# Performance work log

Measured on AMD Instinct MI355X. Metric: run time of the kernel, lower is better.

## Reference

```python
import jax, jax.numpy as jnp
import numpy as np

# DLMLayer (breadth=2) forward, soft/dense path.
# Group arities: 0 (nullary [B,C0]), 1 (unary [B,n,C1]), 2 (binary [B,n,n,C2]).
# Per group i: concat [Expand(inputs[i-1]), inputs[i], Reduce(inputs[i+1])],
# then Permutation(i) (concat over i! axis permutations), then logic MLP
# (Linear -> sigmoid) over the channel dim. exclude_self masks the diagonal
# in the binary->unary reduction (max filled with 0, min filled with 1,
# valid for probabilistic truth values in [0,1]).

def setup_inputs() -> dict:
    key = jax.random.key(0)
    ks = jax.random.split(key, 9)
    B, n, C = 16, 128, 64
    x0 = jax.random.uniform(ks[0], (B, 8), dtype=jnp.float32)
    x1 = jax.random.uniform(ks[1], (B, n, C), dtype=jnp.float32)
    x2 = jax.random.uniform(ks[2], (B, n, n, C), dtype=jnp.float32)
    # current_dim per group: i=0: 8 + 2*64 = 136 ; i=1: 8 + 64 + 2*64 = 200 (1!=1)
    # i=2: (64 + 64) * 2! = 256
    W0 = jax.random.normal(ks[3], (136, C), dtype=jnp.float32) * 0.1
    W1 = jax.random.normal(ks[4], (200, C), dtype=jnp.float32) * 0.1
    W2 = jax.random.normal(ks[5], (256, C), dtype=jnp.float32) * 0.1
    b0 = jnp.zeros((C,), jnp.float32)
    b1 = jnp.zeros((C,), jnp.float32)
    b2 = jnp.zeros((C,), jnp.float32)
    return {"x0": x0, "x1": x1, "x2": x2, "W0": W0, "b0": b0,
            "W1": W1, "b1": b1, "W2": W2, "b2": b2}


def reference(x0, x1, x2, W0, b0, W1, b1, W2, b2):
    B, n, C = x1.shape
    # ---- group 0 (nullary): input x0 + reduce(x1) over the object axis ----
    r1 = jnp.concatenate([x1.max(axis=1), x1.min(axis=1)], axis=-1)  # [B, 2C]
    f0 = jnp.concatenate([x0, r1], axis=-1)                          # [B, 136]
    out0 = jax.nn.sigmoid(f0 @ W0 + b0)                              # [B, C]
    # ---- group 1 (unary): expand x0, input x1, reduce x2 (exclude self) ----
    e0 = jnp.broadcast_to(x0[:, None, :], (B, n, x0.shape[-1]))      # [B, n, 8]
    diag = jnp.eye(n, dtype=bool)[None, :, :, None]                  # [1, n, n, 1]
    rmax = jnp.where(diag, 0.0, x2).max(axis=2)                      # [B, n, C]
    rmin = jnp.where(diag, 1.0, x2).min(axis=2)                      # [B, n, C]
    f1 = jnp.concatenate([e0, x1, rmax, rmin], axis=-1)              # [B, n, 200]
    out1 = jax.nn.sigmoid(f1 @ W1 + b1)                              # [B, n, C]
    # ---- group 2 (binary): expand x1, input x2, permute axes (1,2) ----
    e1 = jnp.broadcast_to(x1[:, :, None, :], (B, n, n, C))           # [B, n, n, C]
    g = jnp.concatenate([e1, x2], axis=-1)                           # [B, n, n, 2C]
    f2 = jnp.concatenate([g, jnp.swapaxes(g, 1, 2)], axis=-1)        # [B, n, n, 4C]
    out2 = jax.nn.sigmoid(f2 @ W2 + b2)                              # [B, n, n, C]
    return (out0, out1, out2)
```

## Files before the change

### kernel.cpp

```cpp
#include <hip/hip_runtime.h>
#include <hip/hip_bf16.h>
#include <cstdint>


#define NDIM 128
#define CDIM 64

typedef float f32x4 __attribute__((ext_vector_type(4)));
typedef short s16x8 __attribute__((ext_vector_type(8)));

__device__ __forceinline__ unsigned short f2bf(float f) {
    union { float f; unsigned int u; } v; v.f = f;
    unsigned int u = v.u;
    return (unsigned short)((u + 0x7FFFu + ((u >> 16) & 1u)) >> 16);
}
__device__ __forceinline__ float sigmoidf_(float x) {
    return 1.0f / (1.0f + __expf(-x));
}
__device__ __forceinline__ uint2 pk4(float4 v) {
    unsigned lo, hi;
    asm("v_cvt_pk_bf16_f32 %0, %1, %2" : "=v"(lo) : "v"(v.x), "v"(v.y));
    asm("v_cvt_pk_bf16_f32 %0, %1, %2" : "=v"(hi) : "v"(v.z), "v"(v.w));
    uint2 r; r.x = lo; r.y = hi; return r;
}

__global__ __launch_bounds__(256) void k_prep(const float* __restrict__ x0,
        const float* __restrict__ x1, const float* __restrict__ W0,
        const float* __restrict__ b0, const float* __restrict__ W2,
        const float* __restrict__ b2, float* __restrict__ PA,
        float* __restrict__ PB, unsigned short* __restrict__ WT,
        float* __restrict__ out0) {
    int bb = blockIdx.x;
    int t = threadIdx.x;
    if (bb < 512) {
        int u = t >> 6, c = t & 63;
        int blk = bb * 4 + u;
        __shared__ float xv[4][64];
        xv[u][c] = x1[blk * 64 + c];
        float accA = b2[c];
        float accB = 0.f;
#pragma unroll 8
        for (int k = 0; k < 64; ++k) {
            float xk = xv[u][k];
            accA += xk * W2[k * 64 + c];
            accB += xk * W2[(128 + k) * 64 + c];
        }
        PA[blk * 64 + c] = accA;
        PB[blk * 64 + c] = accB;
    } else if (bb < 544) {
        int idx = (bb - 512) * 256 + t;
        int n = idx >> 7, k = idx & 127;
        int row = (k < 64) ? (64 + k) : (128 + k);
        WT[idx] = f2bf(W2[row * 64 + n]);
    } else {
        int b = bb - 544;
        int lane = t & 63, w = t >> 6;
        int q = lane & 15;
        int jq = lane >> 4;
        __shared__ float pw[4][64], pn[4][64], f0[136], spart[4][64];
        f32x4 mx = {-1e30f, -1e30f, -1e30f, -1e30f};
        f32x4 mn = {1e30f, 1e30f, 1e30f, 1e30f};
#pragma unroll
        for (int p = 0; p < 8; ++p) {
            int j = (w * 4 + jq) + 16 * p;
            float4 v = *reinterpret_cast<const float4*>(
                x1 + ((size_t)(b * 128 + j)) * 64 + q * 4);
            mx.x = fmaxf(mx.x, v.x); mx.y = fmaxf(mx.y, v.y);
            mx.z = fmaxf(mx.z, v.z); mx.w = fmaxf(mx.w, v.w);
            mn.x = fminf(mn.x, v.x); mn.y = fminf(mn.y, v.y);
            mn.z = fminf(mn.z, v.z); mn.w = fminf(mn.w, v.w);
        }
#pragma unroll
        for (int d = 16; d <= 32; d <<= 1) {
            mx.x = fmaxf(mx.x, __shfl_xor(mx.x, d)); mx.y = fmaxf(mx.y, __shfl_xor(mx.y, d));
            mx.z = fmaxf(mx.z, __shfl_xor(mx.z, d)); mx.w = fmaxf(mx.w, __shfl_xor(mx.w, d));
            mn.x = fminf(mn.x, __shfl_xor(mn.x, d)); mn.y = fminf(mn.y, __shfl_xor(mn.y, d));
            mn.z = fminf(mn.z, __shfl_xor(mn.z, d)); mn.w = fminf(mn.w, __shfl_xor(mn.w, d));
        }
        if (lane < 16) {
            *reinterpret_cast<f32x4*>(&pw[w][lane * 4]) = mx;
            *reinterpret_cast<f32x4*>(&pn[w][lane * 4]) = mn;
        }
        __syncthreads();
        if (t < 64) {
            int c = t;
            float M = fmaxf(fmaxf(pw[0][c], pw[1][c]), fmaxf(pw[2][c], pw[3][c]));
            float m = fminf(fminf(pn[0][c], pn[1][c]), fminf(pn[2][c], pn[3][c]));
            f0[8 + c] = M; f0[72 + c] = m;
            if (c < 8) f0[c] = x0[b * 8 + c];
        }
        __syncthreads();
        {
            int g = t >> 6, c = t & 63;
            float acc = 0.f;
#pragma unroll
            for (int k = g * 34; k < g * 34 + 34; ++k) acc += f0[k] * W0[k * 64 + c];
            spart[g][c] = acc;
        }
        __syncthreads();
        if (t < 64) {
            int c = t;
            out0[b * 64 + c] = sigmoidf_(
                spart[0][c] + spart[1][c] + spart[2][c] + spart[3][c] + b0[c]);
        }
    }
}

__global__ __launch_bounds__(128) void k_main(const float* __restrict__ x2,
        const unsigned short* __restrict__ WT,
        const float* __restrict__ PA, const float* __restrict__ PB,
        float* __restrict__ pmax_ws, float* __restrict__ pmin_ws,
        float* __restrict__ out2) {
    int bid = blockIdx.x;
    int blk = bid >> 1, half = bid & 1;
    int b = blk >> 7, i = blk & 127;
    int j0 = half << 6;
    int t = threadIdx.x;
    int lane = t & 63, w = t >> 6;
    int jq = lane >> 4;
    int cc = (lane & 15) * 4;

    __shared__ __align__(16) unsigned short Ald[64 * 128];

    const float* xaSrc = x2 + (size_t)blk * (NDIM * CDIM);

    float4 va[8];
#pragma unroll
    for (int p = 0; p < 8; ++p) {
        int jl = 32 * w + p * 4 + jq;
        va[p] = *reinterpret_cast<const float4*>(xaSrc + (j0 + jl) * 64 + cc);
    }
    f32x4 mx = {0.f, 0.f, 0.f, 0.f}, mn = {1.f, 1.f, 1.f, 1.f};
#pragma unroll
    for (int p = 0; p < 8; ++p) {
        int jl = 32 * w + p * 4 + jq;
        bool ok = (j0 + jl != i);
        mx.x = fmaxf(mx.x, ok ? va[p].x : 0.0f); mx.y = fmaxf(mx.y, ok ? va[p].y : 0.0f);
        mx.z = fmaxf(mx.z, ok ? va[p].z : 0.0f); mx.w = fmaxf(mx.w, ok ? va[p].w : 0.0f);
        mn.x = fminf(mn.x, ok ? va[p].x : 1.0f); mn.y = fminf(mn.y, ok ? va[p].y : 1.0f);
        mn.z = fminf(mn.z, ok ? va[p].z : 1.0f); mn.w = fminf(mn.w, ok ? va[p].w : 1.0f);
        uint2 u = pk4(va[p]);
        *reinterpret_cast<uint2*>(&Ald[jl * 128 + (cc ^ ((jl & 7) << 3))]) = u;
    }

    float4 vb[8];
#pragma unroll
    for (int p = 0; p < 8; ++p) {
        int jl = 32 * w + p * 4 + jq;
        vb[p] = *reinterpret_cast<const float4*>(
            x2 + ((size_t)((b * 128 + j0 + jl) * 128 + i)) * 64 + cc);
    }

#pragma unroll
    for (int d = 16; d <= 32; d <<= 1) {
        mx.x = fmaxf(mx.x, __shfl_xor(mx.x, d)); mx.y = fmaxf(mx.y, __shfl_xor(mx.y, d));
        mx.z = fmaxf(mx.z, __shfl_xor(mx.z, d)); mx.w = fmaxf(mx.w, __shfl_xor(mx.w, d));
        mn.x = fminf(mn.x, __shfl_xor(mn.x, d)); mn.y = fminf(mn.y, __shfl_xor(mn.y, d));
        mn.z = fminf(mn.z, __shfl_xor(mn.z, d)); mn.w = fminf(mn.w, __shfl_xor(mn.w, d));
    }
    if (lane < 16) {
        int slot = blk * 4 + half * 2 + w;
        *reinterpret_cast<f32x4*>(&pmax_ws[slot * 64 + cc]) = mx;
        *reinterpret_cast<f32x4*>(&pmin_ws[slot * 64 + cc]) = mn;
    }

    s16x8 bf01[2][4];
#pragma unroll
    for (int ks = 0; ks < 2; ++ks)
#pragma unroll
        for (int nt = 0; nt < 4; ++nt) {
            int n = nt * 16 + (lane & 15);
            bf01[ks][nt] = *reinterpret_cast<const s16x8*>(WT + n * 128 + ks * 32 + jq * 8);
        }

    f32x4 acc[2][4];
#pragma unroll
    for (int m = 0; m < 2; ++m)
#pragma unroll
        for (int nt = 0; nt < 4; ++nt) acc[m][nt] = (f32x4){0.f, 0.f, 0.f, 0.f};

    asm volatile("s_waitcnt lgkmcnt(0)" ::: "memory");
    __builtin_amdgcn_sched_barrier(0);

#pragma unroll
    for (int ks = 0; ks < 2; ++ks) {
#pragma unroll
        for (int m = 0; m < 2; ++m) {
            int rowl = 32 * w + m * 16 + (lane & 15);
            int u8 = (ks * 4 + jq) * 8;
            s16x8 afrag = *reinterpret_cast<const s16x8*>(
                &Ald[rowl * 128 + (u8 ^ ((rowl & 7) << 3))]);
#pragma unroll
            for (int nt = 0; nt < 4; ++nt)
                acc[m][nt] = __builtin_amdgcn_mfma_f32_16x16x32_bf16(
                    afrag, bf01[ks][nt], acc[m][nt], 0, 0, 0);
        }
    }

#pragma unroll
    for (int p = 0; p < 8; ++p) {
        int jl = 32 * w + p * 4 + jq;
        uint2 u = pk4(vb[p]);
        *reinterpret_cast<uint2*>(&Ald[jl * 128 + ((64 + cc) ^ ((jl & 7) << 3))]) = u;
    }
    s16x8 bf23[2][4];
#pragma unroll
    for (int ks = 0; ks < 2; ++ks)
#pragma unroll
        for (int nt = 0; nt < 4; ++nt) {
            int n = nt * 16 + (lane & 15);
            bf23[ks][nt] = *reinterpret_cast<const s16x8*>(
                WT + n * 128 + (2 + ks) * 32 + jq * 8);
        }

    asm volatile("s_waitcnt lgkmcnt(0)" ::: "memory");
    __builtin_amdgcn_sched_barrier(0);

#pragma unroll
    for (int ks = 0; ks < 2; ++ks) {
#pragma unroll
        for (int m = 0; m < 2; ++m) {
            int rowl = 32 * w + m * 16 + (lane & 15);
            int u8 = ((2 + ks) * 4 + jq) * 8;
            s16x8 afrag = *reinterpret_cast<const s16x8*>(
                &Ald[rowl * 128 + (u8 ^ ((rowl & 7) << 3))]);
#pragma unroll
            for (int nt = 0; nt < 4; ++nt)
                acc[m][nt] = __builtin_amdgcn_mfma_f32_16x16x32_bf16(
                    afrag, bf23[ks][nt], acc[m][nt], 0, 0, 0);
        }
    }

    const float* PAi = PA + blk * 64;
    const float* PBb = PB + b * 128 * 64;
    float* outBase = out2 + (size_t)blk * (NDIM * CDIM);
#pragma unroll
    for (int m = 0; m < 2; ++m) {
        int jt = j0 + 32 * w + m * 16 + jq * 4;
#pragma unroll
        for (int nt = 0; nt < 4; ++nt) {
            int cp = nt * 16 + (lane & 15);
            float pav = PAi[cp];
#pragma unroll
            for (int r = 0; r < 4; ++r) {
                int j = jt + r;
                outBase[j * 64 + cp] = sigmoidf_(acc[m][nt][r] + pav + PBb[j * 64 + cp]);
            }
        }
    }
}

__global__ __launch_bounds__(256) void k_out1_tail(const float* __restrict__ x0,
        const float* __restrict__ x1, const float* __restrict__ W1,
        const float* __restrict__ b1, const float* __restrict__ pmax_ws,
        const float* __restrict__ pmin_ws, float* __restrict__ out1) {
    int blk = blockIdx.x;
    int t = threadIdx.x;
    int c = t & 63, g = t >> 6;
    __shared__ float sf[200], spart[4][64];
    if (t < 64) {
        float M = 0.f, m = 1.f;
#pragma unroll
        for (int s = 0; s < 4; ++s) {
            M = fmaxf(M, pmax_ws[(blk * 4 + s) * 64 + c]);
            m = fminf(m, pmin_ws[(blk * 4 + s) * 64 + c]);
        }
        sf[72 + c] = M; sf[136 + c] = m;
        sf[8 + c] = x1[blk * 64 + c];
        if (c < 8) sf[c] = x0[(blk >> 7) * 8 + c];
    }
    __syncthreads();
    {
        float a = 0.f;
#pragma unroll 10
        for (int k = g * 50; k < g * 50 + 50; ++k) a += sf[k] * W1[k * 64 + c];
        spart[g][c] = a;
    }
    __syncthreads();
    if (t < 64) {
        out1[blk * 64 + c] = sigmoidf_(
            spart[0][c] + spart[1][c] + spart[2][c] + spart[3][c] + b1[c]);
    }
}

extern "C" void kernel_launch(void* const* d_in, const int* in_sizes, int n_in,
                              void* d_out, int out_size, void* d_ws, size_t ws_size,
                              hipStream_t stream) {
    const float* x0 = (const float*)d_in[0];
    const float* x1 = (const float*)d_in[1];
    const float* x2 = (const float*)d_in[2];
    const float* W0 = (const float*)d_in[3];
    const float* b0 = (const float*)d_in[4];
    const float* W1 = (const float*)d_in[5];
    const float* b1 = (const float*)d_in[6];
    const float* W2 = (const float*)d_in[7];
    const float* b2 = (const float*)d_in[8];

    float* out0 = (float*)d_out;
    float* out1 = out0 + 16 * 64;
    float* out2 = out1 + 16 * 128 * 64;

    float* PA = (float*)d_ws;
    float* PB = PA + 16 * 128 * 64;
    unsigned short* WT = (unsigned short*)(PB + 16 * 128 * 64);
    float* pmax_ws = (float*)(WT + 64 * 128);
    float* pmin_ws = pmax_ws + 2048 * 4 * 64;

    k_prep<<<560, 256, 0, stream>>>(x0, x1, W0, b0, W2, b2, PA, PB, WT, out0);
    k_main<<<4096, 128, 0, stream>>>(x2, WT, PA, PB, pmax_ws, pmin_ws, out2);
    k_out1_tail<<<2048, 256, 0, stream>>>(x0, x1, W1, b1, pmax_ws, pmin_ws, out1);
}
```

Before: 53.30 us.

## Stream transposed x2 tile directly into LDS via global_load_lds

The strided transposed x2 rows (x2[b,j,i,:]) are now loaded with global_load_lds straight into a swizzled fp32 LDS buffer, replacing the register-held vb loads and the later bf16 pack-and-store pass. The bf16 conversion moves to the A-fragment read in the second MFMA half. The intent is to cut register pressure and VGPR round trips and to let the strided gather overlap the first MFMA phase. The cost is a larger LDS footprint (the fp32 buffer) and extra conversions per fragment read. The vmcnt wait with no workgroup barrier before the LDS reads may not be safe with respect to ordering.

```diff
diff --git a/kernel.cpp b/kernel.cpp
--- a/kernel.cpp
+++ b/kernel.cpp
@@ -118,9 +118,11 @@
     int t = threadIdx.x;
     int lane = t & 63, w = t >> 6;
     int jq = lane >> 4;
-    int cc = (lane & 15) * 4;
-
-    __shared__ __align__(16) unsigned short Ald[64 * 128];
+    int l15 = lane & 15;
+    int cc = l15 * 4;
+
+    __shared__ __align__(16) unsigned short Ald[64 * 64];
+    __shared__ __align__(16) float Xb[64 * 64];
 
     const float* xaSrc = x2 + (size_t)blk * (NDIM * CDIM);
 
@@ -130,6 +132,18 @@
         int jl = 32 * w + p * 4 + jq;
         va[p] = *reinterpret_cast<const float4*>(xaSrc + (j0 + jl) * 64 + cc);
     }
+
+#pragma unroll
+    for (int p = 0; p < 8; ++p) {
+        int jl = 32 * w + p * 4 + jq;
+        int scol = (l15 ^ (jl & 7)) * 4;
+        const float* src = x2 + ((size_t)((b * 128 + j0 + jl) * 128 + i)) * 64 + scol;
+        __builtin_amdgcn_global_load_lds(
+            (const __attribute__((address_space(1))) void*)src,
+            (__attribute__((address_space(3))) void*)&Xb[(32 * w + p * 4) * 64],
+            16, 0, 0);
+    }
+
     f32x4 mx = {0.f, 0.f, 0.f, 0.f}, mn = {1.f, 1.f, 1.f, 1.f};
 #pragma unroll
     for (int p = 0; p < 8; ++p) {
@@ -140,15 +154,7 @@
         mn.x = fminf(mn.x, ok ? va[p].x : 1.0f); mn.y = fminf(mn.y, ok ? va[p].y : 1.0f);
         mn.z = fminf(mn.z, ok ? va[p].z : 1.0f); mn.w = fminf(mn.w, ok ? va[p].w : 1.0f);
         uint2 u = pk4(va[p]);
-        *reinterpret_cast<uint2*>(&Ald[jl * 128 + (cc ^ ((jl & 7) << 3))]) = u;
-    }
-
-    float4 vb[8];
-#pragma unroll
-    for (int p = 0; p < 8; ++p) {
-        int jl = 32 * w + p * 4 + jq;
-        vb[p] = *reinterpret_cast<const float4*>(
-            x2 + ((size_t)((b * 128 + j0 + jl) * 128 + i)) * 64 + cc);
+        *reinterpret_cast<uint2*>(&Ald[jl * 64 + (cc ^ ((jl & 7) << 3))]) = u;
     }
 
 #pragma unroll
@@ -169,7 +175,7 @@
     for (int ks = 0; ks < 2; ++ks)
 #pragma unroll
         for (int nt = 0; nt < 4; ++nt) {
-            int n = nt * 16 + (lane & 15);
+            int n = nt * 16 + l15;
             bf01[ks][nt] = *reinterpret_cast<const s16x8*>(WT + n * 128 + ks * 32 + jq * 8);
         }
 
@@ -186,10 +192,9 @@
     for (int ks = 0; ks < 2; ++ks) {
 #pragma unroll
         for (int m = 0; m < 2; ++m) {
-            int rowl = 32 * w + m * 16 + (lane & 15);
-            int u8 = (ks * 4 + jq) * 8;
-            s16x8 afrag = *reinterpret_cast<const s16x8*>(
-                &Ald[rowl * 128 + (u8 ^ ((rowl & 7) << 3))]);
+            int rowl = 32 * w + m * 16 + l15;
+            int u16 = (ks * 32 + jq * 8) ^ ((rowl & 7) << 3);
+            s16x8 afrag = *reinterpret_cast<const s16x8*>(&Ald[rowl * 64 + u16]);
 #pragma unroll
             for (int nt = 0; nt < 4; ++nt)
                 acc[m][nt] = __builtin_amdgcn_mfma_f32_16x16x32_bf16(
@@ -197,37 +202,35 @@
         }
     }
 
-#pragma unroll
-    for (int p = 0; p < 8; ++p) {
-        int jl = 32 * w + p * 4 + jq;
-        uint2 u = pk4(vb[p]);
-        *reinterpret_cast<uint2*>(&Ald[jl * 128 + ((64 + cc) ^ ((jl & 7) << 3))]) = u;
-    }
     s16x8 bf23[2][4];
 #pragma unroll
     for (int ks = 0; ks < 2; ++ks)
 #pragma unroll
         for (int nt = 0; nt < 4; ++nt) {
-            int n = nt * 16 + (lane & 15);
+            int n = nt * 16 + l15;
             bf23[ks][nt] = *reinterpret_cast<const s16x8*>(
                 WT + n * 128 + (2 + ks) * 32 + jq * 8);
         }
 
-    asm volatile("s_waitcnt lgkmcnt(0)" ::: "memory");
+    asm volatile("s_waitcnt vmcnt(0)" ::: "memory");
     __builtin_amdgcn_sched_barrier(0);
-
 #pragma unroll
     for (int ks = 0; ks < 2; ++ks) {
 #pragma unroll
         for (int m = 0; m < 2; ++m) {
-            int rowl = 32 * w + m * 16 + (lane & 15);
-            int u8 = ((2 + ks) * 4 + jq) * 8;
-            s16x8 afrag = *reinterpret_cast<const s16x8*>(
-                &Ald[rowl * 128 + (u8 ^ ((rowl & 7) << 3))]);
+            int rowl = 32 * w + m * 16 + l15;
+            int sw = (rowl & 7) << 2;
+            int base = ks * 32 + jq * 8;
+            f32x4 xlo = *reinterpret_cast<const f32x4*>(&Xb[rowl * 64 + ((base) ^ sw)]);
+            f32x4 xhi = *reinterpret_cast<const f32x4*>(&Xb[rowl * 64 + ((base + 4) ^ sw)]);
+            uint2 plo = pk4(float4{xlo[0], xlo[1], xlo[2], xlo[3]});
+            uint2 phi = pk4(float4{xhi[0], xhi[1], xhi[2], xhi[3]});
+            union { unsigned u[4]; s16x8 v; } fr;
+            fr.u[0] = plo.x; fr.u[1] = plo.y; fr.u[2] = phi.x; fr.u[3] = phi.y;
 #pragma unroll
             for (int nt = 0; nt < 4; ++nt)
                 acc[m][nt] = __builtin_amdgcn_mfma_f32_16x16x32_bf16(
-                    afrag, bf23[ks][nt], acc[m][nt], 0, 0, 0);
+                    fr.v, bf23[ks][nt], acc[m][nt], 0, 0, 0);
         }
     }
 
@@ -239,7 +242,7 @@
         int jt = j0 + 32 * w + m * 16 + jq * 4;
 #pragma unroll
         for (int nt = 0; nt < 4; ++nt) {
-            int cp = nt * 16 + (lane & 15);
+            int cp = nt * 16 + l15;
             float pav = PAi[cp];
 #pragma unroll
             for (int r = 0; r < 4; ++r) {
```

After: 58.07 us. +8.9%, slower.

## Process four tiles per block in k_main with next-tile prefetch

Applied to the files above, without the earlier changes.

k_main now loops over four consecutive (b,i,half) tiles per block, which cuts the grid from 4096 to 1024 blocks. During each iteration it issues the next tile's row loads from x2 early, so global load latency overlaps the current tile's MFMA work and output stores. This spends fewer blocks on launch and prologue cost. In exchange, the device has far fewer resident waves to hide memory latency on what is largely a bandwidth-bound kernel, and register pressure rises from the extra prefetch buffers.

```diff
diff --git a/kernel.cpp b/kernel.cpp
--- a/kernel.cpp
+++ b/kernel.cpp
@@ -111,140 +111,157 @@
         const float* __restrict__ PA, const float* __restrict__ PB,
         float* __restrict__ pmax_ws, float* __restrict__ pmin_ws,
         float* __restrict__ out2) {
-    int bid = blockIdx.x;
-    int blk = bid >> 1, half = bid & 1;
-    int b = blk >> 7, i = blk & 127;
-    int j0 = half << 6;
     int t = threadIdx.x;
     int lane = t & 63, w = t >> 6;
     int jq = lane >> 4;
-    int cc = (lane & 15) * 4;
+    int l15 = lane & 15;
+    int cc = l15 * 4;
+    int bid4 = blockIdx.x << 2;
 
     __shared__ __align__(16) unsigned short Ald[64 * 128];
 
-    const float* xaSrc = x2 + (size_t)blk * (NDIM * CDIM);
-
-    float4 va[8];
-#pragma unroll
-    for (int p = 0; p < 8; ++p) {
-        int jl = 32 * w + p * 4 + jq;
-        va[p] = *reinterpret_cast<const float4*>(xaSrc + (j0 + jl) * 64 + cc);
-    }
-    f32x4 mx = {0.f, 0.f, 0.f, 0.f}, mn = {1.f, 1.f, 1.f, 1.f};
-#pragma unroll
-    for (int p = 0; p < 8; ++p) {
-        int jl = 32 * w + p * 4 + jq;
-        bool ok = (j0 + jl != i);
-        mx.x = fmaxf(mx.x, ok ? va[p].x : 0.0f); mx.y = fmaxf(mx.y, ok ? va[p].y : 0.0f);
-        mx.z = fmaxf(mx.z, ok ? va[p].z : 0.0f); mx.w = fmaxf(mx.w, ok ? va[p].w : 0.0f);
-        mn.x = fminf(mn.x, ok ? va[p].x : 1.0f); mn.y = fminf(mn.y, ok ? va[p].y : 1.0f);
-        mn.z = fminf(mn.z, ok ? va[p].z : 1.0f); mn.w = fminf(mn.w, ok ? va[p].w : 1.0f);
-        uint2 u = pk4(va[p]);
-        *reinterpret_cast<uint2*>(&Ald[jl * 128 + (cc ^ ((jl & 7) << 3))]) = u;
-    }
-
-    float4 vb[8];
-#pragma unroll
-    for (int p = 0; p < 8; ++p) {
-        int jl = 32 * w + p * 4 + jq;
-        vb[p] = *reinterpret_cast<const float4*>(
-            x2 + ((size_t)((b * 128 + j0 + jl) * 128 + i)) * 64 + cc);
-    }
-
-#pragma unroll
-    for (int d = 16; d <= 32; d <<= 1) {
-        mx.x = fmaxf(mx.x, __shfl_xor(mx.x, d)); mx.y = fmaxf(mx.y, __shfl_xor(mx.y, d));
-        mx.z = fmaxf(mx.z, __shfl_xor(mx.z, d)); mx.w = fmaxf(mx.w, __shfl_xor(mx.w, d));
-        mn.x = fminf(mn.x, __shfl_xor(mn.x, d)); mn.y = fminf(mn.y, __shfl_xor(mn.y, d));
-        mn.z = fminf(mn.z, __shfl_xor(mn.z, d)); mn.w = fminf(mn.w, __shfl_xor(mn.w, d));
-    }
-    if (lane < 16) {
-        int slot = blk * 4 + half * 2 + w;
-        *reinterpret_cast<f32x4*>(&pmax_ws[slot * 64 + cc]) = mx;
-        *reinterpret_cast<f32x4*>(&pmin_ws[slot * 64 + cc]) = mn;
-    }
-
-    s16x8 bf01[2][4];
-#pragma unroll
-    for (int ks = 0; ks < 2; ++ks)
-#pragma unroll
-        for (int nt = 0; nt < 4; ++nt) {
-            int n = nt * 16 + (lane & 15);
-            bf01[ks][nt] = *reinterpret_cast<const s16x8*>(WT + n * 128 + ks * 32 + jq * 8);
-        }
-
-    f32x4 acc[2][4];
-#pragma unroll
-    for (int m = 0; m < 2; ++m)
-#pragma unroll
-        for (int nt = 0; nt < 4; ++nt) acc[m][nt] = (f32x4){0.f, 0.f, 0.f, 0.f};
-
-    asm volatile("s_waitcnt lgkmcnt(0)" ::: "memory");
-    __builtin_amdgcn_sched_barrier(0);
-
-#pragma unroll
-    for (int ks = 0; ks < 2; ++ks) {
+    float4 vaP[8];
+    {
+        int blk2 = bid4;
+        int blk = blk2 >> 1, half = blk2 & 1;
+        const float* xaSrc = x2 + (size_t)blk * (NDIM * CDIM) + ((half << 6) * 64);
+#pragma unroll
+        for (int p = 0; p < 8; ++p) {
+            int jl = 32 * w + p * 4 + jq;
+            vaP[p] = *reinterpret_cast<const float4*>(xaSrc + jl * 64 + cc);
+        }
+    }
+
+#pragma unroll
+    for (int u = 0; u < 4; ++u) {
+        int blk2 = bid4 + u;
+        int blk = blk2 >> 1, half = blk2 & 1;
+        int b = blk >> 7, i = blk & 127;
+        int j0 = half << 6;
+
+        float4 vb[8];
+#pragma unroll
+        for (int p = 0; p < 8; ++p) {
+            int jl = 32 * w + p * 4 + jq;
+            vb[p] = *reinterpret_cast<const float4*>(
+                x2 + ((size_t)((b * 128 + j0 + jl) * 128 + i)) * 64 + cc);
+        }
+
+        f32x4 mx = {0.f, 0.f, 0.f, 0.f}, mn = {1.f, 1.f, 1.f, 1.f};
+#pragma unroll
+        for (int p = 0; p < 8; ++p) {
+            int jl = 32 * w + p * 4 + jq;
+            bool ok = (j0 + jl != i);
+            mx.x = fmaxf(mx.x, ok ? vaP[p].x : 0.0f); mx.y = fmaxf(mx.y, ok ? vaP[p].y : 0.0f);
+            mx.z = fmaxf(mx.z, ok ? vaP[p].z : 0.0f); mx.w = fmaxf(mx.w, ok ? vaP[p].w : 0.0f);
+            mn.x = fminf(mn.x, ok ? vaP[p].x : 1.0f); mn.y = fminf(mn.y, ok ? vaP[p].y : 1.0f);
+            mn.z = fminf(mn.z, ok ? vaP[p].z : 1.0f); mn.w = fminf(mn.w, ok ? vaP[p].w : 1.0f);
+            uint2 uu = pk4(vaP[p]);
+            *reinterpret_cast<uint2*>(&Ald[jl * 128 + (cc ^ ((jl & 7) << 3))]) = uu;
+        }
+#pragma unroll
+        for (int d = 16; d <= 32; d <<= 1) {
+            mx.x = fmaxf(mx.x, __shfl_xor(mx.x, d)); mx.y = fmaxf(mx.y, __shfl_xor(mx.y, d));
+            mx.z = fmaxf(mx.z, __shfl_xor(mx.z, d)); mx.w = fmaxf(mx.w, __shfl_xor(mx.w, d));
+            mn.x = fminf(mn.x, __shfl_xor(mn.x, d)); mn.y = fminf(mn.y, __shfl_xor(mn.y, d));
+            mn.z = fminf(mn.z, __shfl_xor(mn.z, d)); mn.w = fminf(mn.w, __shfl_xor(mn.w, d));
+        }
+        if (lane < 16) {
+            int slot = blk * 4 + half * 2 + w;
+            *reinterpret_cast<f32x4*>(&pmax_ws[slot * 64 + cc]) = mx;
+            *reinterpret_cast<f32x4*>(&pmin_ws[slot * 64 + cc]) = mn;
+        }
+
+        if (u < 3) {
+            int nblk2 = bid4 + u + 1;
+            int nblk = nblk2 >> 1, nhalf = nblk2 & 1;
+            const float* nsrc = x2 + (size_t)nblk * (NDIM * CDIM) + ((nhalf << 6) * 64);
+#pragma unroll
+            for (int p = 0; p < 8; ++p) {
+                int jl = 32 * w + p * 4 + jq;
+                vaP[p] = *reinterpret_cast<const float4*>(nsrc + jl * 64 + cc);
+            }
+        }
+
+#pragma unroll
+        for (int p = 0; p < 8; ++p) {
+            int jl = 32 * w + p * 4 + jq;
+            uint2 uu = pk4(vb[p]);
+            *reinterpret_cast<uint2*>(&Ald[jl * 128 + ((64 + cc) ^ ((jl & 7) << 3))]) = uu;
+        }
+
+        f32x4 acc[2][4];
+#pragma unroll
+        for (int m = 0; m < 2; ++m)
+#pragma unroll
+            for (int nt = 0; nt < 4; ++nt) acc[m][nt] = (f32x4){0.f, 0.f, 0.f, 0.f};
+
+        s16x8 bf01[2][4];
+#pragma unroll
+        for (int ks = 0; ks < 2; ++ks)
+#pragma unroll
+            for (int nt = 0; nt < 4; ++nt) {
+                int n = nt * 16 + l15;
+                bf01[ks][nt] = *reinterpret_cast<const s16x8*>(
+                    WT + n * 128 + ks * 32 + jq * 8);
+            }
+
+        asm volatile("s_waitcnt lgkmcnt(0)" ::: "memory");
+        __builtin_amdgcn_sched_barrier(0);
+
+#pragma unroll
+        for (int ks = 0; ks < 2; ++ks) {
+#pragma unroll
+            for (int m = 0; m < 2; ++m) {
+                int rowl = 32 * w + m * 16 + l15;
+                int u8 = (ks * 4 + jq) * 8;
+                s16x8 afrag = *reinterpret_cast<const s16x8*>(
+                    &Ald[rowl * 128 + (u8 ^ ((rowl & 7) << 3))]);
+#pragma unroll
+                for (int nt = 0; nt < 4; ++nt)
+                    acc[m][nt] = __builtin_amdgcn_mfma_f32_16x16x32_bf16(
+                        afrag, bf01[ks][nt], acc[m][nt], 0, 0, 0);
+            }
+        }
+        s16x8 bf23[2][4];
+#pragma unroll
+        for (int ks = 0; ks < 2; ++ks)
+#pragma unroll
+            for (int nt = 0; nt < 4; ++nt) {
+                int n = nt * 16 + l15;
+                bf23[ks][nt] = *reinterpret_cast<const s16x8*>(
+                    WT + n * 128 + (2 + ks) * 32 + jq * 8);
+            }
+#pragma unroll
+        for (int ks = 0; ks < 2; ++ks) {
+#pragma unroll
+            for (int m = 0; m < 2; ++m) {
+                int rowl = 32 * w + m * 16 + l15;
+                int u8 = ((2 + ks) * 4 + jq) * 8;
+                s16x8 afrag = *reinterpret_cast<const s16x8*>(
+                    &Ald[rowl * 128 + (u8 ^ ((rowl & 7) << 3))]);
+#pragma unroll
+                for (int nt = 0; nt < 4; ++nt)
+                    acc[m][nt] = __builtin_amdgcn_mfma_f32_16x16x32_bf16(
+                        afrag, bf23[ks][nt], acc[m][nt], 0, 0, 0);
+            }
+        }
+
+        const float* PAi = PA + blk * 64;
+        const float* PBb = PB + b * 128 * 64;
+        float* outBase = out2 + (size_t)blk * (NDIM * CDIM);
 #pragma unroll
         for (int m = 0; m < 2; ++m) {
-            int rowl = 32 * w + m * 16 + (lane & 15);
-            int u8 = (ks * 4 + jq) * 8;
-            s16x8 afrag = *reinterpret_cast<const s16x8*>(
-                &Ald[rowl * 128 + (u8 ^ ((rowl & 7) << 3))]);
-#pragma unroll
-            for (int nt = 0; nt < 4; ++nt)
-                acc[m][nt] = __builtin_amdgcn_mfma_f32_16x16x32_bf16(
-                    afrag, bf01[ks][nt], acc[m][nt], 0, 0, 0);
-        }
-    }
-
-#pragma unroll
-    for (int p = 0; p < 8; ++p) {
-        int jl = 32 * w + p * 4 + jq;
-        uint2 u = pk4(vb[p]);
-        *reinterpret_cast<uint2*>(&Ald[jl * 128 + ((64 + cc) ^ ((jl & 7) << 3))]) = u;
-    }
-    s16x8 bf23[2][4];
-#pragma unroll
-    for (int ks = 0; ks < 2; ++ks)
-#pragma unroll
-        for (int nt = 0; nt < 4; ++nt) {
-            int n = nt * 16 + (lane & 15);
-            bf23[ks][nt] = *reinterpret_cast<const s16x8*>(
-                WT + n * 128 + (2 + ks) * 32 + jq * 8);
-        }
-
-    asm volatile("s_waitcnt lgkmcnt(0)" ::: "memory");
-    __builtin_amdgcn_sched_barrier(0);
-
-#pragma unroll
-    for (int ks = 0; ks < 2; ++ks) {
-#pragma unroll
-        for (int m = 0; m < 2; ++m) {
-            int rowl = 32 * w + m * 16 + (lane & 15);
-            int u8 = ((2 + ks) * 4 + jq) * 8;
-            s16x8 afrag = *reinterpret_cast<const s16x8*>(
-                &Ald[rowl * 128 + (u8 ^ ((rowl & 7) << 3))]);
-#pragma unroll
-            for (int nt = 0; nt < 4; ++nt)
-                acc[m][nt] = __builtin_amdgcn_mfma_f32_16x16x32_bf16(
-                    afrag, bf23[ks][nt], acc[m][nt], 0, 0, 0);
-        }
-    }
-
-    const float* PAi = PA + blk * 64;
-    const float* PBb = PB + b * 128 * 64;
-    float* outBase = out2 + (size_t)blk * (NDIM * CDIM);
-#pragma unroll
-    for (int m = 0; m < 2; ++m) {
-        int jt = j0 + 32 * w + m * 16 + jq * 4;
-#pragma unroll
-        for (int nt = 0; nt < 4; ++nt) {
-            int cp = nt * 16 + (lane & 15);
-            float pav = PAi[cp];
-#pragma unroll
-            for (int r = 0; r < 4; ++r) {
-                int j = jt + r;
-                outBase[j * 64 + cp] = sigmoidf_(acc[m][nt][r] + pav + PBb[j * 64 + cp]);
+            int jt = j0 + 32 * w + m * 16 + jq * 4;
+#pragma unroll
+            for (int nt = 0; nt < 4; ++nt) {
+                int cp = nt * 16 + l15;
+                float pav = PAi[cp];
+#pragma unroll
+                for (int r = 0; r < 4; ++r) {
+                    int j = jt + r;
+                    outBase[j * 64 + cp] = sigmoidf_(acc[m][nt][r] + pav + PBb[j * 64 + cp]);
+                }
             }
         }
     }
@@ -307,6 +324,6 @@
     float* pmin_ws = pmax_ws + 2048 * 4 * 64;
 
     k_prep<<<560, 256, 0, stream>>>(x0, x1, W0, b0, W2, b2, PA, PB, WT, out0);
-    k_main<<<4096, 128, 0, stream>>>(x2, WT, PA, PB, pmax_ws, pmin_ws, out2);
+    k_main<<<1024, 128, 0, stream>>>(x2, WT, PA, PB, pmax_ws, pmin_ws, out2);
     k_out1_tail<<<2048, 256, 0, stream>>>(x0, x1, W1, b1, pmax_ws, pmin_ws, out1);
 }
```

Result: slower. 84.61 us (+58.7%).
